# Performance work log

Measured on AMD Instinct MI355X. Metric: run time of the kernel, lower is better.

## Reference

```python
import jax, jax.numpy as jnp
import numpy as np

N = 20000          # nodes
E = 200000         # edges
IN = 256           # in_channels
OUT = 256          # out_channels (heads * per-head)
H = 2              # heads
C = OUT // 2       # per-head channels (out_channels // 2)
TDIM = 100         # time_enc.out_channels
MSG = 156          # msg_dim
EDGE_DIM = TDIM + MSG  # 256
P = 0.1            # dropout prob


def setup_inputs() -> dict:
    key = jax.random.key(0)
    ks = jax.random.split(key, 20)
    s = 1.0 / np.sqrt(IN)
    se = 1.0 / np.sqrt(EDGE_DIM)
    return {
        "x": jax.random.normal(ks[0], (N, IN), jnp.float32),
        "last_update": jax.random.uniform(ks[1], (N,), jnp.float32) * 100.0,
        "edge_index": jax.random.randint(ks[2], (2, E), 0, N, jnp.int64),
        "t": jax.random.uniform(ks[3], (E,), jnp.float32) * 100.0,
        "msg": jax.random.normal(ks[4], (E, MSG), jnp.float32),
        "u_edge": jax.random.uniform(ks[5], (E,), jnp.float32),
        "u_attn": jax.random.uniform(ks[6], (E, H), jnp.float32),
        # TimeEncoder: cos(Linear(1, TDIM))
        "time_w": jax.random.normal(ks[7], (TDIM,), jnp.float32),
        "time_b": jax.random.normal(ks[8], (TDIM,), jnp.float32) * 0.1,
        # TransformerConv params ([in, out] layout)
        "Wq": jax.random.normal(ks[9], (IN, H * C), jnp.float32) * s,
        "bq": jnp.zeros((H * C,), jnp.float32),
        "Wk": jax.random.normal(ks[10], (IN, H * C), jnp.float32) * s,
        "bk": jnp.zeros((H * C,), jnp.float32),
        "Wv": jax.random.normal(ks[11], (IN, H * C), jnp.float32) * s,
        "bv": jnp.zeros((H * C,), jnp.float32),
        "We": jax.random.normal(ks[12], (EDGE_DIM, H * C), jnp.float32) * se,
        "be": jnp.zeros((H * C,), jnp.float32),
        "Ws": jax.random.normal(ks[13], (IN, H * C), jnp.float32) * s,
        "bs": jnp.zeros((H * C,), jnp.float32),
    }


def reference(x, last_update, edge_index, t, msg, u_edge, u_attn,
              time_w, time_b, Wq, bq, Wk, bk, Wv, bv, We, be, Ws, bs):
    src, dst = edge_index[0], edge_index[1]
    # time encoding of relative time (TGN TimeEncoder: cos(Linear(1, TDIM)))
    rel_t = last_update[src] - t                              # [E]
    rel_enc = jnp.cos(rel_t[:, None] * time_w[None, :] + time_b)  # [E, TDIM]
    edge_attr = jnp.concatenate([rel_enc, msg], axis=-1)      # [E, EDGE_DIM]
    # dropout_adj: drop edges with prob P (no rescale)
    keep = u_edge > P                                         # [E] bool

    q = (x @ Wq + bq).reshape(N, H, C)
    k = (x @ Wk + bk).reshape(N, H, C)
    v = (x @ Wv + bv).reshape(N, H, C)
    e = (edge_attr @ We + be).reshape(E, H, C)

    kj = k[src] + e                                           # [E, H, C]
    alpha = jnp.einsum('ehc,ehc->eh', q[dst], kj) / jnp.sqrt(jnp.float32(C))
    alpha = jnp.where(keep[:, None], alpha, -jnp.inf)
    # segment softmax over incoming edges of each dst node
    m = jax.ops.segment_max(alpha, dst, num_segments=N)       # [N, H]
    m = jnp.where(jnp.isfinite(m), m, 0.0)
    ex = jnp.where(keep[:, None], jnp.exp(alpha - m[dst]), 0.0)
    denom = jax.ops.segment_sum(ex, dst, num_segments=N)      # [N, H]
    attn = ex / (denom[dst] + 1e-16)                          # [E, H]
    # attention dropout (post-softmax, inverted scaling)
    attn = attn * (u_attn > P).astype(attn.dtype) / (1.0 - P)

    msg_out = (v[src] + e) * attn[:, :, None]                 # [E, H, C]
    out = jax.ops.segment_sum(msg_out, dst, num_segments=N).reshape(N, H * C)
    # root/skip connection
    return out + (x @ Ws + bs)
```

## Files before the change

### kernel.cpp

```cpp
#include <hip/hip_runtime.h>

#define NND 20000
#define NE 200000
#define PDROP 0.1f

typedef unsigned short u16;
typedef __bf16 bf16x8 __attribute__((ext_vector_type(8)));
typedef float f32x4 __attribute__((ext_vector_type(4)));

__device__ __forceinline__ float b2f(u16 u) {
  unsigned v = ((unsigned)u) << 16;
  float f;
  __builtin_memcpy(&f, &v, 4);
  return f;
}
__device__ __forceinline__ u16 f2b(float f) {
  unsigned x;
  __builtin_memcpy(&x, &f, 4);
  unsigned r = x + 0x7fffu + ((x >> 16) & 1u);
  return (u16)(r >> 16);
}

__global__ void convert_x(const float* __restrict__ x, u16* __restrict__ xb) {
  int i = blockIdx.x * blockDim.x + threadIdx.x;
  if (i < NND * 256 / 4) {
    float4 v = ((const float4*)x)[i];
    ushort4 o;
    o.x = f2b(v.x); o.y = f2b(v.y); o.z = f2b(v.z); o.w = f2b(v.w);
    ((ushort4*)xb)[i] = o;
  }
}

struct WTArgs {
  const float* W[6];
  u16* WT[6];
};
__global__ void convert_wT(WTArgs a) {
  int gid = blockIdx.x * blockDim.x + threadIdx.x;
  if (gid >= 6 * 65536) return;
  int w = gid >> 16, r = gid & 65535;
  if (w < 5) {
    int n = r >> 8, k = r & 255;
    a.WT[w][n * 256 + k] = f2b(a.W[w][k * 256 + n]);
  } else {
    a.WT[5][r] = f2b(a.W[5][r]);
  }
}

__global__ void build_relt(const float* __restrict__ last_update,
                           const int* __restrict__ ei, const float* __restrict__ t,
                           float* __restrict__ relt) {
  int e = blockIdx.x * blockDim.x + threadIdx.x;
  if (e < NE) relt[e] = last_update[ei[e]] - t[e];
}

__global__ void zero2(int* __restrict__ cnt, int* __restrict__ cur) {
  int i = blockIdx.x * blockDim.x + threadIdx.x;
  if (i < NND) { cnt[i] = 0; cur[i] = 0; }
}
__global__ void csr_count(const int* __restrict__ ei, int* __restrict__ cnt) {
  int e = blockIdx.x * blockDim.x + threadIdx.x;
  if (e < NE) atomicAdd(&cnt[ei[NE + e]], 1);
}
__global__ __launch_bounds__(1024) void scan_rowptr(const int* __restrict__ cnt,
                                                    int* __restrict__ rowptr) {
  __shared__ int sums[1024];
  const int tid = threadIdx.x;
  const int base = tid * 20;
  int local[20];
  int run = 0;
#pragma unroll
  for (int i = 0; i < 20; i++) {
    int idx = base + i;
    local[i] = run;
    run += (idx < NND) ? cnt[idx] : 0;
  }
  sums[tid] = run;
  __syncthreads();
  for (int off = 1; off < 1024; off <<= 1) {
    int v = (tid >= off) ? sums[tid - off] : 0;
    __syncthreads();
    sums[tid] += v;
    __syncthreads();
  }
  int prev = (tid > 0) ? sums[tid - 1] : 0;
#pragma unroll
  for (int i = 0; i < 20; i++) {
    int idx = base + i;
    if (idx < NND) rowptr[idx] = prev + local[i];
  }
  if (tid == 1023) rowptr[NND] = sums[1023];
}
__global__ void csr_fill(const int* __restrict__ ei, const int* __restrict__ rowptr,
                         int* __restrict__ cur, int* __restrict__ elist) {
  int e = blockIdx.x * blockDim.x + threadIdx.x;
  if (e < NE) {
    int d = ei[NE + e];
    int pos = rowptr[d] + atomicAdd(&cur[d], 1);
    elist[pos] = e;
  }
}

__device__ __forceinline__ void mfma_tile(const u16 (*As)[72], const u16 (*Bs)[72],
                                          f32x4 acc[4][4], int wm, int wn,
                                          int fr, int fg) {
#pragma unroll
  for (int ks = 0; ks < 2; ks++) {
    bf16x8 a[4], b[4];
#pragma unroll
    for (int i = 0; i < 4; i++)
      a[i] = *(const bf16x8*)&As[wm * 64 + i * 16 + fr][ks * 32 + fg * 8];
#pragma unroll
    for (int j = 0; j < 4; j++)
      b[j] = *(const bf16x8*)&Bs[wn * 64 + j * 16 + fr][ks * 32 + fg * 8];
#pragma unroll
    for (int i = 0; i < 4; i++)
#pragma unroll
      for (int j = 0; j < 4; j++)
        acc[i][j] = __builtin_amdgcn_mfma_f32_16x16x32_bf16(a[i], b[j], acc[i][j], 0, 0, 0);
  }
}

struct NodeArgs {
  const u16* BT[4];
  const float* bias[4];
  u16* outb[3];
  float* outf;
};
__global__ __launch_bounds__(256) void gemm_node(const u16* __restrict__ xb,
                                                 NodeArgs args) {
  __shared__ __attribute__((aligned(16))) u16 As[128][72];
  __shared__ __attribute__((aligned(16))) u16 Bs[128][72];
  const int tid = threadIdx.x;
  const int w = blockIdx.y >> 1;
  const int col0 = (blockIdx.y & 1) * 128;
  const int row0 = blockIdx.x * 128;
  const u16* BT = args.BT[w];
  const float* bias = args.bias[w];
  const int wid = tid >> 6, lane = tid & 63;
  const int wm = wid >> 1, wn = wid & 1;
  const int fr = lane & 15, fg = lane >> 4;
  f32x4 acc[4][4] = {};
  for (int k0 = 0; k0 < 256; k0 += 64) {
#pragma unroll
    for (int i = 0; i < 4; i++) {
      int idx = tid + i * 256;
      int row = idx >> 3, vc = idx & 7;
      int g = row0 + row;
      uint4 v = make_uint4(0, 0, 0, 0);
      if (g < NND) v = *(const uint4*)&xb[(size_t)g * 256 + k0 + vc * 8];
      *(uint4*)&As[row][vc * 8] = v;
      *(uint4*)&Bs[row][vc * 8] = *(const uint4*)&BT[(size_t)(col0 + row) * 256 + k0 + vc * 8];
    }
    __syncthreads();
    mfma_tile(As, Bs, acc, wm, wn, fr, fg);
    __syncthreads();
  }
#pragma unroll
  for (int mi = 0; mi < 4; mi++) {
#pragma unroll
    for (int rr = 0; rr < 4; rr++) {
      int grow = row0 + wm * 64 + mi * 16 + fg * 4 + rr;
      if (grow >= NND) continue;
#pragma unroll
      for (int ni = 0; ni < 4; ni++) {
        int gcol = col0 + wn * 64 + ni * 16 + fr;
        float val = acc[mi][ni][rr] + bias[gcol];
        if (w < 3)
          args.outb[w][(size_t)grow * 256 + gcol] = f2b(val);
        else
          args.outf[(size_t)grow * 256 + gcol] = val;
      }
    }
  }
}

__global__ __launch_bounds__(256) void gemm_qwe(const u16* __restrict__ qb,
                                                const u16* __restrict__ Web,
                                                u16* __restrict__ qWeb) {
  __shared__ __attribute__((aligned(16))) u16 As[128][72];
  __shared__ __attribute__((aligned(16))) u16 Bs[128][72];
  const int tid = threadIdx.x;
  const int h = blockIdx.y >> 1;
  const int col0 = (blockIdx.y & 1) * 128;
  const int row0 = blockIdx.x * 128;
  const int wid = tid >> 6, lane = tid & 63;
  const int wm = wid >> 1, wn = wid & 1;
  const int fr = lane & 15, fg = lane >> 4;
  f32x4 acc[4][4] = {};
  for (int k0 = 0; k0 < 128; k0 += 64) {
#pragma unroll
    for (int i = 0; i < 4; i++) {
      int idx = tid + i * 256;
      int row = idx >> 3, vc = idx & 7;
      int g = row0 + row;
      uint4 v = make_uint4(0, 0, 0, 0);
      if (g < NND) v = *(const uint4*)&qb[(size_t)g * 256 + h * 128 + k0 + vc * 8];
      *(uint4*)&As[row][vc * 8] = v;
      *(uint4*)&Bs[row][vc * 8] =
          *(const uint4*)&Web[(size_t)(col0 + row) * 256 + h * 128 + k0 + vc * 8];
    }
    __syncthreads();
    mfma_tile(As, Bs, acc, wm, wn, fr, fg);
    __syncthreads();
  }
#pragma unroll
  for (int mi = 0; mi < 4; mi++) {
#pragma unroll
    for (int rr = 0; rr < 4; rr++) {
      int grow = row0 + wm * 64 + mi * 16 + fg * 4 + rr;
      if (grow >= NND) continue;
#pragma unroll
      for (int ni = 0; ni < 4; ni++) {
        int gj = col0 + wn * 64 + ni * 16 + fr;
        qWeb[(size_t)grow * 512 + h * 256 + gj] = f2b(acc[mi][ni][rr]);
      }
    }
  }
}

__global__ __launch_bounds__(256) void node_fused(
    const u16* __restrict__ qb, const u16* __restrict__ kb,
    const u16* __restrict__ vb, const u16* __restrict__ qWeb,
    const int* __restrict__ ei, const int* __restrict__ rowptr,
    const int* __restrict__ elist, const float* __restrict__ relt,
    const float* __restrict__ msg, const float* __restrict__ tw,
    const float* __restrict__ tb, const float* __restrict__ be,
    const float* __restrict__ u_edge, const float* __restrict__ u_attn,
    float* __restrict__ alphabuf, u16* __restrict__ aggb,
    float* __restrict__ out) {
  const int node = (blockIdx.x * blockDim.x + threadIdx.x) >> 6;
  const int lane = threadIdx.x & 63;
  const int c0 = lane * 4;
  const int hl = lane >> 5;
  const int beg = rowptr[node], end = rowptr[node + 1];

  ushort4 q4 = *(const ushort4*)&qb[(size_t)node * 256 + c0];
  float qf0 = b2f(q4.x), qf1 = b2f(q4.y), qf2 = b2f(q4.z), qf3 = b2f(q4.w);
  ushort4 w0v = *(const ushort4*)&qWeb[(size_t)node * 512 + c0];
  ushort4 w1v = *(const ushort4*)&qWeb[(size_t)node * 512 + 256 + c0];
  float qw00 = b2f(w0v.x), qw01 = b2f(w0v.y), qw02 = b2f(w0v.z), qw03 = b2f(w0v.w);
  float qw10 = b2f(w1v.x), qw11 = b2f(w1v.y), qw12 = b2f(w1v.z), qw13 = b2f(w1v.w);
  float4 bev = *(const float4*)&be[c0];
  float pb = qf0 * bev.x + qf1 * bev.y + qf2 * bev.z + qf3 * bev.w;
#pragma unroll
  for (int off = 16; off; off >>= 1) pb += __shfl_xor(pb, off);
  float tw0 = 0, tw1 = 0, tw2 = 0, tw3 = 0, tb0 = 0, tb1 = 0, tb2 = 0, tb3 = 0;
  if (c0 < 100) {
    float4 a = *(const float4*)&tw[c0];
    float4 b = *(const float4*)&tb[c0];
    tw0 = a.x; tw1 = a.y; tw2 = a.z; tw3 = a.w;
    tb0 = b.x; tb1 = b.y; tb2 = b.z; tb3 = b.w;
  }
  const float inv = 0.08838834764831845f;

  float m = -INFINITY;
  for (int j = beg; j < end; ++j) {
    int eid = elist[j];
    int s = ei[eid];
    float rt = relt[eid];
    ushort4 k4 = *(const ushort4*)&kb[(size_t)s * 256 + c0];
    float pqk = qf0 * b2f(k4.x) + qf1 * b2f(k4.y) + qf2 * b2f(k4.z) + qf3 * b2f(k4.w);
    float ea0, ea1, ea2, ea3;
    if (c0 < 100) {
      ea0 = __cosf(rt * tw0 + tb0); ea1 = __cosf(rt * tw1 + tb1);
      ea2 = __cosf(rt * tw2 + tb2); ea3 = __cosf(rt * tw3 + tb3);
    } else {
      float4 mm = *(const float4*)&msg[(size_t)eid * 156 + (c0 - 100)];
      ea0 = mm.x; ea1 = mm.y; ea2 = mm.z; ea3 = mm.w;
    }
    float pe0 = qw00 * ea0 + qw01 * ea1 + qw02 * ea2 + qw03 * ea3;
    float pe1 = qw10 * ea0 + qw11 * ea1 + qw12 * ea2 + qw13 * ea3;
    float y0 = pe0 + __shfl_xor(pe0, 32);
    float y1 = pe1 + __shfl_xor(pe1, 32);
    float z = (lane < 32) ? y0 : y1;
#pragma unroll
    for (int off = 16; off; off >>= 1) {
      z += __shfl_xor(z, off);
      pqk += __shfl_xor(pqk, off);
    }
    bool keep = u_edge[eid] > PDROP;
    float a = keep ? (pqk + z + pb) * inv : -INFINITY;
    m = fmaxf(m, a);
    alphabuf[2 * j + hl] = a;
  }

  float den = 0.f, sw = 0.f;
  float vc0 = 0, vc1 = 0, vc2 = 0, vc3 = 0;
  float g00 = 0, g01 = 0, g02 = 0, g03 = 0;
  float g10 = 0, g11 = 0, g12 = 0, g13 = 0;
  for (int j = beg; j < end; ++j) {
    int eid = elist[j];
    float a = alphabuf[2 * j + hl];
    float ex = (a > -1e30f) ? __expf(a - m) : 0.f;
    den += ex;
    float wa = ex * ((u_attn[(size_t)eid * 2 + hl] > PDROP) ? (1.f / 0.9f) : 0.f);
    float wo = __shfl_xor(wa, 32);
    float w0 = (lane < 32) ? wa : wo;
    float w1 = (lane < 32) ? wo : wa;
    if (w0 + w1 != 0.f) {
      int s = ei[eid];
      float rt = relt[eid];
      ushort4 v4 = *(const ushort4*)&vb[(size_t)s * 256 + c0];
      float ea0, ea1, ea2, ea3;
      if (c0 < 100) {
        ea0 = __cosf(rt * tw0 + tb0); ea1 = __cosf(rt * tw1 + tb1);
        ea2 = __cosf(rt * tw2 + tb2); ea3 = __cosf(rt * tw3 + tb3);
      } else {
        float4 mm = *(const float4*)&msg[(size_t)eid * 156 + (c0 - 100)];
        ea0 = mm.x; ea1 = mm.y; ea2 = mm.z; ea3 = mm.w;
      }
      vc0 += wa * b2f(v4.x); vc1 += wa * b2f(v4.y);
      vc2 += wa * b2f(v4.z); vc3 += wa * b2f(v4.w);
      g00 += w0 * ea0; g01 += w0 * ea1; g02 += w0 * ea2; g03 += w0 * ea3;
      g10 += w1 * ea0; g11 += w1 * ea1; g12 += w1 * ea2; g13 += w1 * ea3;
      sw += wa;
    }
  }
  float rden = 1.f / (den + 1e-16f);
  float ro = __shfl_xor(rden, 32);
  float r0 = (lane < 32) ? rden : ro;
  float r1 = (lane < 32) ? ro : rden;
  float4 o = *(float4*)&out[(size_t)node * 256 + c0];
  o.x += (vc0 + sw * bev.x) * rden;
  o.y += (vc1 + sw * bev.y) * rden;
  o.z += (vc2 + sw * bev.z) * rden;
  o.w += (vc3 + sw * bev.w) * rden;
  *(float4*)&out[(size_t)node * 256 + c0] = o;
  ushort4 a0, a1;
  a0.x = f2b(g00 * r0); a0.y = f2b(g01 * r0); a0.z = f2b(g02 * r0); a0.w = f2b(g03 * r0);
  a1.x = f2b(g10 * r1); a1.y = f2b(g11 * r1); a1.z = f2b(g12 * r1); a1.w = f2b(g13 * r1);
  *(ushort4*)&aggb[(size_t)node * 256 + c0] = a0;
  *(ushort4*)&aggb[(size_t)(NND + node) * 256 + c0] = a1;
}

__global__ __launch_bounds__(256) void gemm_final(const u16* __restrict__ aggb,
                                                  const u16* __restrict__ WeT,
                                                  float* __restrict__ out) {
  __shared__ __attribute__((aligned(16))) u16 As[128][72];
  __shared__ __attribute__((aligned(16))) u16 Bs[128][72];
  const int tid = threadIdx.x;
  const int h = blockIdx.y;
  const int row0 = blockIdx.x * 128;
  const u16* A = aggb + (size_t)h * NND * 256;
  const int wid = tid >> 6, lane = tid & 63;
  const int wm = wid >> 1, wn = wid & 1;
  const int fr = lane & 15, fg = lane >> 4;
  f32x4 acc[4][4] = {};
  for (int k0 = 0; k0 < 256; k0 += 64) {
#pragma unroll
    for (int i = 0; i < 4; i++) {
      int idx = tid + i * 256;
      int row = idx >> 3, vc = idx & 7;
      int g = row0 + row;
      uint4 v = make_uint4(0, 0, 0, 0);
      if (g < NND) v = *(const uint4*)&A[(size_t)g * 256 + k0 + vc * 8];
      *(uint4*)&As[row][vc * 8] = v;
      *(uint4*)&Bs[row][vc * 8] =
          *(const uint4*)&WeT[(size_t)(h * 128 + row) * 256 + k0 + vc * 8];
    }
    __syncthreads();
    mfma_tile(As, Bs, acc, wm, wn, fr, fg);
    __syncthreads();
  }
#pragma unroll
  for (int mi = 0; mi < 4; mi++) {
#pragma unroll
    for (int rr = 0; rr < 4; rr++) {
      int grow = row0 + wm * 64 + mi * 16 + fg * 4 + rr;
      if (grow >= NND) continue;
#pragma unroll
      for (int ni = 0; ni < 4; ni++) {
        int gcol = wn * 64 + ni * 16 + fr;
        out[(size_t)grow * 256 + h * 128 + gcol] += acc[mi][ni][rr];
      }
    }
  }
}

extern "C" void kernel_launch(void* const* d_in, const int* in_sizes, int n_in,
                              void* d_out, int out_size, void* d_ws, size_t ws_size,
                              hipStream_t stream) {
  const float* x = (const float*)d_in[0];
  const float* last_update = (const float*)d_in[1];
  const int* ei = (const int*)d_in[2];
  const float* t = (const float*)d_in[3];
  const float* msg = (const float*)d_in[4];
  const float* u_edge = (const float*)d_in[5];
  const float* u_attn = (const float*)d_in[6];
  const float* time_w = (const float*)d_in[7];
  const float* time_b = (const float*)d_in[8];
  const float* Wq = (const float*)d_in[9];
  const float* bq = (const float*)d_in[10];
  const float* Wk = (const float*)d_in[11];
  const float* bk = (const float*)d_in[12];
  const float* Wv = (const float*)d_in[13];
  const float* bv = (const float*)d_in[14];
  const float* We = (const float*)d_in[15];
  const float* be = (const float*)d_in[16];
  const float* Ws = (const float*)d_in[17];
  const float* bs = (const float*)d_in[18];
  float* out = (float*)d_out;

  char* ws = (char*)d_ws;
  u16* xb = (u16*)(ws + 0);
  u16* WT0 = (u16*)(ws + 10240000);
  float* relt = (float*)(ws + 11026432);
  u16* qb = (u16*)(ws + 11826432);
  u16* kb = (u16*)(ws + 22066432);
  u16* vb = (u16*)(ws + 32306432);
  u16* qWeb = (u16*)(ws + 42546432);
  u16* aggb = (u16*)(ws + 63026432);
  float* alphabuf = (float*)(ws + 83506432);
  int* cnt = (int*)(ws + 85106432);
  int* cur = (int*)(ws + 85186432);
  int* rowptr = (int*)(ws + 85266432);
  int* elist = (int*)(ws + 85346448);

  zero2<<<(NND + 255) / 256, 256, 0, stream>>>(cnt, cur);
  csr_count<<<(NE + 255) / 256, 256, 0, stream>>>(ei, cnt);
  scan_rowptr<<<1, 1024, 0, stream>>>(cnt, rowptr);
  csr_fill<<<(NE + 255) / 256, 256, 0, stream>>>(ei, rowptr, cur, elist);

  WTArgs wa;
  wa.W[0] = Wq; wa.W[1] = Wk; wa.W[2] = Wv; wa.W[3] = Ws; wa.W[4] = We; wa.W[5] = We;
  for (int i = 0; i < 6; i++) wa.WT[i] = WT0 + (size_t)i * 65536;
  convert_wT<<<(6 * 65536 + 255) / 256, 256, 0, stream>>>(wa);
  convert_x<<<(NND * 64 + 255) / 256, 256, 0, stream>>>(x, xb);
  build_relt<<<(NE + 255) / 256, 256, 0, stream>>>(last_update, ei, t, relt);

  NodeArgs na;
  na.BT[0] = wa.WT[0]; na.BT[1] = wa.WT[1]; na.BT[2] = wa.WT[2]; na.BT[3] = wa.WT[3];
  na.bias[0] = bq; na.bias[1] = bk; na.bias[2] = bv; na.bias[3] = bs;
  na.outb[0] = qb; na.outb[1] = kb; na.outb[2] = vb;
  na.outf = out;
  dim3 gn((NND + 127) / 128, 8);
  gemm_node<<<gn, 256, 0, stream>>>(xb, na);

  dim3 gq((NND + 127) / 128, 4);
  gemm_qwe<<<gq, 256, 0, stream>>>(qb, wa.WT[5], qWeb);

  node_fused<<<NND / 4, 256, 0, stream>>>(qb, kb, vb, qWeb, ei, rowptr, elist,
                                          relt, msg, time_w, time_b, be, u_edge,
                                          u_attn, alphabuf, aggb, out);

  dim3 gf((NND + 127) / 128, 2);
  gemm_final<<<gf, 256, 0, stream>>>(aggb, wa.WT[4], out);
}
```

Before: 286.9 us.

## Split node-fused attention into edge-parallel alpha kernel and node aggregation

Replaces the per-node fused kernel with an edge-parallel kernel that computes attention logits one wavefront per edge and scatters them, along with dropout masks, relative time and source ids, into CSR order. A node-level kernel then does the segment softmax and aggregation from these compacted arrays and reads a bf16 copy of msg. The aim is to remove the load imbalance and serial per-node logit loop of the old kernel and to make the aggregation reads contiguous. In exchange it adds an extra kernel launch, extra workspace traffic for the scattered arrays and the bf16 msg copy, and bf16 rounding of msg.

```diff
diff --git a/kernel.cpp b/kernel.cpp
--- a/kernel.cpp
+++ b/kernel.cpp
@@ -47,13 +47,6 @@
   }
 }
 
-__global__ void build_relt(const float* __restrict__ last_update,
-                           const int* __restrict__ ei, const float* __restrict__ t,
-                           float* __restrict__ relt) {
-  int e = blockIdx.x * blockDim.x + threadIdx.x;
-  if (e < NE) relt[e] = last_update[ei[e]] - t[e];
-}
-
 __global__ void zero2(int* __restrict__ cnt, int* __restrict__ cur) {
   int i = blockIdx.x * blockDim.x + threadIdx.x;
   if (i < NND) { cnt[i] = 0; cur[i] = 0; }
@@ -92,12 +85,14 @@
   if (tid == 1023) rowptr[NND] = sums[1023];
 }
 __global__ void csr_fill(const int* __restrict__ ei, const int* __restrict__ rowptr,
-                         int* __restrict__ cur, int* __restrict__ elist) {
+                         int* __restrict__ cur, int* __restrict__ elist,
+                         int* __restrict__ pos) {
   int e = blockIdx.x * blockDim.x + threadIdx.x;
   if (e < NE) {
     int d = ei[NE + e];
-    int pos = rowptr[d] + atomicAdd(&cur[d], 1);
-    elist[pos] = e;
+    int p = rowptr[d] + atomicAdd(&cur[d], 1);
+    elist[p] = e;
+    pos[e] = p;
   }
 }
 
@@ -219,117 +214,139 @@
   }
 }
 
-__global__ __launch_bounds__(256) void node_fused(
+__global__ __launch_bounds__(256) void edge_alpha(
     const u16* __restrict__ qb, const u16* __restrict__ kb,
-    const u16* __restrict__ vb, const u16* __restrict__ qWeb,
-    const int* __restrict__ ei, const int* __restrict__ rowptr,
-    const int* __restrict__ elist, const float* __restrict__ relt,
+    const u16* __restrict__ qWeb, const int* __restrict__ ei,
+    const float* __restrict__ last_update, const float* __restrict__ t,
     const float* __restrict__ msg, const float* __restrict__ tw,
-    const float* __restrict__ tb, const float* __restrict__ be,
+    const float* __restrict__ tb_, const float* __restrict__ be,
     const float* __restrict__ u_edge, const float* __restrict__ u_attn,
-    float* __restrict__ alphabuf, u16* __restrict__ aggb,
+    const int* __restrict__ pos, float2* __restrict__ alpha2,
+    float2* __restrict__ wm2, float* __restrict__ reltc,
+    int* __restrict__ srcc, u16* __restrict__ msgb) {
+  int e = (blockIdx.x * blockDim.x + threadIdx.x) >> 6;
+  int lane = threadIdx.x & 63;
+  if (e >= NE) return;
+  int c0 = lane * 4;
+  int s = ei[e], d = ei[NE + e];
+  float rt = last_update[s] - t[e];
+  ushort4 q4 = *(const ushort4*)&qb[(size_t)d * 256 + c0];
+  ushort4 k4 = *(const ushort4*)&kb[(size_t)s * 256 + c0];
+  float4 bev = *(const float4*)&be[c0];
+  float pqk = b2f(q4.x) * (b2f(k4.x) + bev.x) + b2f(q4.y) * (b2f(k4.y) + bev.y) +
+              b2f(q4.z) * (b2f(k4.z) + bev.z) + b2f(q4.w) * (b2f(k4.w) + bev.w);
+  float ea0, ea1, ea2, ea3;
+  if (c0 < 100) {
+    float4 a = *(const float4*)&tw[c0];
+    float4 b = *(const float4*)&tb_[c0];
+    ea0 = __cosf(rt * a.x + b.x); ea1 = __cosf(rt * a.y + b.y);
+    ea2 = __cosf(rt * a.z + b.z); ea3 = __cosf(rt * a.w + b.w);
+  } else {
+    float4 mm = *(const float4*)&msg[(size_t)e * 156 + (c0 - 100)];
+    ea0 = mm.x; ea1 = mm.y; ea2 = mm.z; ea3 = mm.w;
+    ushort4 mo;
+    mo.x = f2b(ea0); mo.y = f2b(ea1); mo.z = f2b(ea2); mo.w = f2b(ea3);
+    *(ushort4*)&msgb[(size_t)e * 156 + (c0 - 100)] = mo;
+  }
+  ushort4 w0v = *(const ushort4*)&qWeb[(size_t)d * 512 + c0];
+  ushort4 w1v = *(const ushort4*)&qWeb[(size_t)d * 512 + 256 + c0];
+  float pe0 = b2f(w0v.x) * ea0 + b2f(w0v.y) * ea1 + b2f(w0v.z) * ea2 + b2f(w0v.w) * ea3;
+  float pe1 = b2f(w1v.x) * ea0 + b2f(w1v.y) * ea1 + b2f(w1v.z) * ea2 + b2f(w1v.w) * ea3;
+  float y0 = pe0 + __shfl_xor(pe0, 32);
+  float y1 = pe1 + __shfl_xor(pe1, 32);
+  float z = (lane < 32) ? y0 : y1;
+#pragma unroll
+  for (int off = 16; off; off >>= 1) {
+    z += __shfl_xor(z, off);
+    pqk += __shfl_xor(pqk, off);
+  }
+  float a = (pqk + z) * 0.08838834764831845f;
+  if (!(u_edge[e] > PDROP)) a = -INFINITY;
+  float aothr = __shfl_xor(a, 32);
+  if (lane == 0) {
+    int p = pos[e];
+    alpha2[p] = make_float2(a, aothr);
+    float2 ua = *(const float2*)&u_attn[(size_t)e * 2];
+    wm2[p] = make_float2(ua.x > PDROP ? (1.f / 0.9f) : 0.f,
+                         ua.y > PDROP ? (1.f / 0.9f) : 0.f);
+    reltc[p] = rt;
+    srcc[p] = s;
+  }
+}
+
+__global__ __launch_bounds__(256) void node_agg(
+    const u16* __restrict__ vb, const u16* __restrict__ msgb,
+    const float2* __restrict__ alpha2, const float2* __restrict__ wm2,
+    const float* __restrict__ reltc, const int* __restrict__ srcc,
+    const int* __restrict__ elist, const int* __restrict__ rowptr,
+    const float* __restrict__ tw, const float* __restrict__ tb_,
+    const float* __restrict__ be, u16* __restrict__ aggb,
     float* __restrict__ out) {
-  const int node = (blockIdx.x * blockDim.x + threadIdx.x) >> 6;
-  const int lane = threadIdx.x & 63;
-  const int c0 = lane * 4;
-  const int hl = lane >> 5;
+  int node = (blockIdx.x * blockDim.x + threadIdx.x) >> 6;
+  int lane = threadIdx.x & 63;
+  if (node >= NND) return;
   const int beg = rowptr[node], end = rowptr[node + 1];
-
-  ushort4 q4 = *(const ushort4*)&qb[(size_t)node * 256 + c0];
-  float qf0 = b2f(q4.x), qf1 = b2f(q4.y), qf2 = b2f(q4.z), qf3 = b2f(q4.w);
-  ushort4 w0v = *(const ushort4*)&qWeb[(size_t)node * 512 + c0];
-  ushort4 w1v = *(const ushort4*)&qWeb[(size_t)node * 512 + 256 + c0];
-  float qw00 = b2f(w0v.x), qw01 = b2f(w0v.y), qw02 = b2f(w0v.z), qw03 = b2f(w0v.w);
-  float qw10 = b2f(w1v.x), qw11 = b2f(w1v.y), qw12 = b2f(w1v.z), qw13 = b2f(w1v.w);
-  float4 bev = *(const float4*)&be[c0];
-  float pb = qf0 * bev.x + qf1 * bev.y + qf2 * bev.z + qf3 * bev.w;
-#pragma unroll
-  for (int off = 16; off; off >>= 1) pb += __shfl_xor(pb, off);
+  const int c0 = lane * 4, hl = lane >> 5;
   float tw0 = 0, tw1 = 0, tw2 = 0, tw3 = 0, tb0 = 0, tb1 = 0, tb2 = 0, tb3 = 0;
   if (c0 < 100) {
     float4 a = *(const float4*)&tw[c0];
-    float4 b = *(const float4*)&tb[c0];
+    float4 b = *(const float4*)&tb_[c0];
     tw0 = a.x; tw1 = a.y; tw2 = a.z; tw3 = a.w;
     tb0 = b.x; tb1 = b.y; tb2 = b.z; tb3 = b.w;
   }
-  const float inv = 0.08838834764831845f;
-
-  float m = -INFINITY;
+  float4 bev = *(const float4*)&be[c0];
+  float m0 = -INFINITY, m1 = -INFINITY;
   for (int j = beg; j < end; ++j) {
-    int eid = elist[j];
-    int s = ei[eid];
-    float rt = relt[eid];
-    ushort4 k4 = *(const ushort4*)&kb[(size_t)s * 256 + c0];
-    float pqk = qf0 * b2f(k4.x) + qf1 * b2f(k4.y) + qf2 * b2f(k4.z) + qf3 * b2f(k4.w);
-    float ea0, ea1, ea2, ea3;
-    if (c0 < 100) {
-      ea0 = __cosf(rt * tw0 + tb0); ea1 = __cosf(rt * tw1 + tb1);
-      ea2 = __cosf(rt * tw2 + tb2); ea3 = __cosf(rt * tw3 + tb3);
-    } else {
-      float4 mm = *(const float4*)&msg[(size_t)eid * 156 + (c0 - 100)];
-      ea0 = mm.x; ea1 = mm.y; ea2 = mm.z; ea3 = mm.w;
-    }
-    float pe0 = qw00 * ea0 + qw01 * ea1 + qw02 * ea2 + qw03 * ea3;
-    float pe1 = qw10 * ea0 + qw11 * ea1 + qw12 * ea2 + qw13 * ea3;
-    float y0 = pe0 + __shfl_xor(pe0, 32);
-    float y1 = pe1 + __shfl_xor(pe1, 32);
-    float z = (lane < 32) ? y0 : y1;
-#pragma unroll
-    for (int off = 16; off; off >>= 1) {
-      z += __shfl_xor(z, off);
-      pqk += __shfl_xor(pqk, off);
-    }
-    bool keep = u_edge[eid] > PDROP;
-    float a = keep ? (pqk + z + pb) * inv : -INFINITY;
-    m = fmaxf(m, a);
-    alphabuf[2 * j + hl] = a;
-  }
-
-  float den = 0.f, sw = 0.f;
+    float2 a2 = alpha2[j];
+    m0 = fmaxf(m0, a2.x);
+    m1 = fmaxf(m1, a2.y);
+  }
+  float den0 = 0.f, den1 = 0.f, sw0 = 0.f, sw1 = 0.f;
   float vc0 = 0, vc1 = 0, vc2 = 0, vc3 = 0;
   float g00 = 0, g01 = 0, g02 = 0, g03 = 0;
   float g10 = 0, g11 = 0, g12 = 0, g13 = 0;
   for (int j = beg; j < end; ++j) {
-    int eid = elist[j];
-    float a = alphabuf[2 * j + hl];
-    float ex = (a > -1e30f) ? __expf(a - m) : 0.f;
-    den += ex;
-    float wa = ex * ((u_attn[(size_t)eid * 2 + hl] > PDROP) ? (1.f / 0.9f) : 0.f);
-    float wo = __shfl_xor(wa, 32);
-    float w0 = (lane < 32) ? wa : wo;
-    float w1 = (lane < 32) ? wo : wa;
+    float2 a2 = alpha2[j];
+    float ex0 = (a2.x > -1e30f) ? __expf(a2.x - m0) : 0.f;
+    float ex1 = (a2.y > -1e30f) ? __expf(a2.y - m1) : 0.f;
+    den0 += ex0; den1 += ex1;
+    float2 wm = wm2[j];
+    float w0 = ex0 * wm.x, w1 = ex1 * wm.y;
     if (w0 + w1 != 0.f) {
-      int s = ei[eid];
-      float rt = relt[eid];
+      int s = srcc[j];
+      float rt = reltc[j];
       ushort4 v4 = *(const ushort4*)&vb[(size_t)s * 256 + c0];
       float ea0, ea1, ea2, ea3;
       if (c0 < 100) {
         ea0 = __cosf(rt * tw0 + tb0); ea1 = __cosf(rt * tw1 + tb1);
         ea2 = __cosf(rt * tw2 + tb2); ea3 = __cosf(rt * tw3 + tb3);
       } else {
-        float4 mm = *(const float4*)&msg[(size_t)eid * 156 + (c0 - 100)];
-        ea0 = mm.x; ea1 = mm.y; ea2 = mm.z; ea3 = mm.w;
+        int eid = elist[j];
+        ushort4 mm = *(const ushort4*)&msgb[(size_t)eid * 156 + (c0 - 100)];
+        ea0 = b2f(mm.x); ea1 = b2f(mm.y); ea2 = b2f(mm.z); ea3 = b2f(mm.w);
       }
-      vc0 += wa * b2f(v4.x); vc1 += wa * b2f(v4.y);
-      vc2 += wa * b2f(v4.z); vc3 += wa * b2f(v4.w);
+      float wv = hl ? w1 : w0;
+      vc0 += wv * b2f(v4.x); vc1 += wv * b2f(v4.y);
+      vc2 += wv * b2f(v4.z); vc3 += wv * b2f(v4.w);
       g00 += w0 * ea0; g01 += w0 * ea1; g02 += w0 * ea2; g03 += w0 * ea3;
       g10 += w1 * ea0; g11 += w1 * ea1; g12 += w1 * ea2; g13 += w1 * ea3;
-      sw += wa;
-    }
-  }
-  float rden = 1.f / (den + 1e-16f);
-  float ro = __shfl_xor(rden, 32);
-  float r0 = (lane < 32) ? rden : ro;
-  float r1 = (lane < 32) ? ro : rden;
+      sw0 += w0; sw1 += w1;
+    }
+  }
+  float rden0 = 1.f / (den0 + 1e-16f), rden1 = 1.f / (den1 + 1e-16f);
+  float rv = hl ? rden1 : rden0;
+  float swv = hl ? sw1 : sw0;
   float4 o = *(float4*)&out[(size_t)node * 256 + c0];
-  o.x += (vc0 + sw * bev.x) * rden;
-  o.y += (vc1 + sw * bev.y) * rden;
-  o.z += (vc2 + sw * bev.z) * rden;
-  o.w += (vc3 + sw * bev.w) * rden;
+  o.x += (vc0 + swv * bev.x) * rv;
+  o.y += (vc1 + swv * bev.y) * rv;
+  o.z += (vc2 + swv * bev.z) * rv;
+  o.w += (vc3 + swv * bev.w) * rv;
   *(float4*)&out[(size_t)node * 256 + c0] = o;
   ushort4 a0, a1;
-  a0.x = f2b(g00 * r0); a0.y = f2b(g01 * r0); a0.z = f2b(g02 * r0); a0.w = f2b(g03 * r0);
-  a1.x = f2b(g10 * r1); a1.y = f2b(g11 * r1); a1.z = f2b(g12 * r1); a1.w = f2b(g13 * r1);
+  a0.x = f2b(g00 * rden0); a0.y = f2b(g01 * rden0);
+  a0.z = f2b(g02 * rden0); a0.w = f2b(g03 * rden0);
+  a1.x = f2b(g10 * rden1); a1.y = f2b(g11 * rden1);
+  a1.z = f2b(g12 * rden1); a1.w = f2b(g13 * rden1);
   *(ushort4*)&aggb[(size_t)node * 256 + c0] = a0;
   *(ushort4*)&aggb[(size_t)(NND + node) * 256 + c0] = a1;
 }
@@ -405,29 +422,32 @@
   char* ws = (char*)d_ws;
   u16* xb = (u16*)(ws + 0);
   u16* WT0 = (u16*)(ws + 10240000);
-  float* relt = (float*)(ws + 11026432);
-  u16* qb = (u16*)(ws + 11826432);
-  u16* kb = (u16*)(ws + 22066432);
-  u16* vb = (u16*)(ws + 32306432);
-  u16* qWeb = (u16*)(ws + 42546432);
-  u16* aggb = (u16*)(ws + 63026432);
-  float* alphabuf = (float*)(ws + 83506432);
-  int* cnt = (int*)(ws + 85106432);
-  int* cur = (int*)(ws + 85186432);
-  int* rowptr = (int*)(ws + 85266432);
-  int* elist = (int*)(ws + 85346448);
+  u16* qb = (u16*)(ws + 11026432);
+  u16* kb = (u16*)(ws + 21266432);
+  u16* vb = (u16*)(ws + 31506432);
+  u16* qWeb = (u16*)(ws + 41746432);
+  u16* aggb = (u16*)(ws + 62226432);
+  float2* alpha2 = (float2*)(ws + 82706432);
+  float2* wm2 = (float2*)(ws + 84306432);
+  float* reltc = (float*)(ws + 85906432);
+  int* srcc = (int*)(ws + 86706432);
+  int* pos = (int*)(ws + 87506432);
+  int* elist = (int*)(ws + 88306432);
+  u16* msgb = (u16*)(ws + 89106432);
+  int* cnt = (int*)(ws + 151506432);
+  int* cur = (int*)(ws + 151586432);
+  int* rowptr = (int*)(ws + 151666432);
 
   zero2<<<(NND + 255) / 256, 256, 0, stream>>>(cnt, cur);
   csr_count<<<(NE + 255) / 256, 256, 0, stream>>>(ei, cnt);
   scan_rowptr<<<1, 1024, 0, stream>>>(cnt, rowptr);
-  csr_fill<<<(NE + 255) / 256, 256, 0, stream>>>(ei, rowptr, cur, elist);
+  csr_fill<<<(NE + 255) / 256, 256, 0, stream>>>(ei, rowptr, cur, elist, pos);
 
   WTArgs wa;
   wa.W[0] = Wq; wa.W[1] = Wk; wa.W[2] = Wv; wa.W[3] = Ws; wa.W[4] = We; wa.W[5] = We;
   for (int i = 0; i < 6; i++) wa.WT[i] = WT0 + (size_t)i * 65536;
   convert_wT<<<(6 * 65536 + 255) / 256, 256, 0, stream>>>(wa);
   convert_x<<<(NND * 64 + 255) / 256, 256, 0, stream>>>(x, xb);
-  build_relt<<<(NE + 255) / 256, 256, 0, stream>>>(last_update, ei, t, relt);
 
   NodeArgs na;
   na.BT[0] = wa.WT[0]; na.BT[1] = wa.WT[1]; na.BT[2] = wa.WT[2]; na.BT[3] = wa.WT[3];
@@ -440,9 +460,13 @@
   dim3 gq((NND + 127) / 128, 4);
   gemm_qwe<<<gq, 256, 0, stream>>>(qb, wa.WT[5], qWeb);
 
-  node_fused<<<NND / 4, 256, 0, stream>>>(qb, kb, vb, qWeb, ei, rowptr, elist,
-                                          relt, msg, time_w, time_b, be, u_edge,
-                                          u_attn, alphabuf, aggb, out);
+  edge_alpha<<<(NE + 3) / 4, 256, 0, stream>>>(
+      qb, kb, qWeb, ei, last_update, t, msg, time_w, time_b, be, u_edge,
+      u_attn, pos, alpha2, wm2, reltc, srcc, msgb);
+
+  node_agg<<<(NND + 3) / 4, 256, 0, stream>>>(
+      vb, msgb, alpha2, wm2, reltc, srcc, elist, rowptr, time_w, time_b, be,
+      aggb, out);
 
   dim3 gf((NND + 127) / 128, 2);
   gemm_final<<<gf, 256, 0, stream>>>(aggb, wa.WT[4], out);
```

Result: slower. 333.1 us (+16.1%).

## Fuse two-pass segment softmax into single online-softmax pass and inline rel_t

Applied to the files above, without the earlier changes.

Replaces the two-pass per-node softmax (score pass writing alphabuf, then a weighted-accumulate pass re-reading edges) with a single online-softmax loop that rescales the running accumulators whenever the per-head max grows. The edge's time-encoding cos values and msg loads are now computed once instead of twice, the alphabuf round-trip is removed, and the build_relt kernel is dropped by computing last_update[src]-t inline. In exchange, every edge now loads v and u_attn even when it is dropped, and the loop does extra exp and rescale work.

```diff
diff --git a/kernel.cpp b/kernel.cpp
--- a/kernel.cpp
+++ b/kernel.cpp
@@ -47,13 +47,6 @@
   }
 }
 
-__global__ void build_relt(const float* __restrict__ last_update,
-                           const int* __restrict__ ei, const float* __restrict__ t,
-                           float* __restrict__ relt) {
-  int e = blockIdx.x * blockDim.x + threadIdx.x;
-  if (e < NE) relt[e] = last_update[ei[e]] - t[e];
-}
-
 __global__ void zero2(int* __restrict__ cnt, int* __restrict__ cur) {
   int i = blockIdx.x * blockDim.x + threadIdx.x;
   if (i < NND) { cnt[i] = 0; cur[i] = 0; }
@@ -96,8 +89,8 @@
   int e = blockIdx.x * blockDim.x + threadIdx.x;
   if (e < NE) {
     int d = ei[NE + e];
-    int pos = rowptr[d] + atomicAdd(&cur[d], 1);
-    elist[pos] = e;
+    int p = rowptr[d] + atomicAdd(&cur[d], 1);
+    elist[p] = e;
   }
 }
 
@@ -222,18 +215,18 @@
 __global__ __launch_bounds__(256) void node_fused(
     const u16* __restrict__ qb, const u16* __restrict__ kb,
     const u16* __restrict__ vb, const u16* __restrict__ qWeb,
-    const int* __restrict__ ei, const int* __restrict__ rowptr,
-    const int* __restrict__ elist, const float* __restrict__ relt,
-    const float* __restrict__ msg, const float* __restrict__ tw,
-    const float* __restrict__ tb, const float* __restrict__ be,
-    const float* __restrict__ u_edge, const float* __restrict__ u_attn,
-    float* __restrict__ alphabuf, u16* __restrict__ aggb,
+    const int* __restrict__ ei, const float* __restrict__ last_update,
+    const float* __restrict__ t, const float* __restrict__ msg,
+    const float* __restrict__ tw, const float* __restrict__ tb_,
+    const float* __restrict__ be, const float* __restrict__ u_edge,
+    const float* __restrict__ u_attn, const int* __restrict__ rowptr,
+    const int* __restrict__ elist, u16* __restrict__ aggb,
     float* __restrict__ out) {
   const int node = (blockIdx.x * blockDim.x + threadIdx.x) >> 6;
   const int lane = threadIdx.x & 63;
-  const int c0 = lane * 4;
-  const int hl = lane >> 5;
+  if (node >= NND) return;
   const int beg = rowptr[node], end = rowptr[node + 1];
+  const int c0 = lane * 4, hl = lane >> 5;
 
   ushort4 q4 = *(const ushort4*)&qb[(size_t)node * 256 + c0];
   float qf0 = b2f(q4.x), qf1 = b2f(q4.y), qf2 = b2f(q4.z), qf3 = b2f(q4.w);
@@ -248,19 +241,26 @@
   float tw0 = 0, tw1 = 0, tw2 = 0, tw3 = 0, tb0 = 0, tb1 = 0, tb2 = 0, tb3 = 0;
   if (c0 < 100) {
     float4 a = *(const float4*)&tw[c0];
-    float4 b = *(const float4*)&tb[c0];
+    float4 b = *(const float4*)&tb_[c0];
     tw0 = a.x; tw1 = a.y; tw2 = a.z; tw3 = a.w;
     tb0 = b.x; tb1 = b.y; tb2 = b.z; tb3 = b.w;
   }
   const float inv = 0.08838834764831845f;
 
-  float m = -INFINITY;
+  float m0 = -INFINITY, m1 = -INFINITY;
+  float den0 = 0.f, den1 = 0.f, sw0 = 0.f, sw1 = 0.f;
+  float vc0 = 0, vc1 = 0, vc2 = 0, vc3 = 0;
+  float g00 = 0, g01 = 0, g02 = 0, g03 = 0;
+  float g10 = 0, g11 = 0, g12 = 0, g13 = 0;
+
   for (int j = beg; j < end; ++j) {
     int eid = elist[j];
     int s = ei[eid];
-    float rt = relt[eid];
+    float rt = last_update[s] - t[eid];
     ushort4 k4 = *(const ushort4*)&kb[(size_t)s * 256 + c0];
-    float pqk = qf0 * b2f(k4.x) + qf1 * b2f(k4.y) + qf2 * b2f(k4.z) + qf3 * b2f(k4.w);
+    ushort4 v4 = *(const ushort4*)&vb[(size_t)s * 256 + c0];
+    bool keep = u_edge[eid] > PDROP;
+    float2 ua = *(const float2*)&u_attn[(size_t)eid * 2];
     float ea0, ea1, ea2, ea3;
     if (c0 < 100) {
       ea0 = __cosf(rt * tw0 + tb0); ea1 = __cosf(rt * tw1 + tb1);
@@ -269,6 +269,7 @@
       float4 mm = *(const float4*)&msg[(size_t)eid * 156 + (c0 - 100)];
       ea0 = mm.x; ea1 = mm.y; ea2 = mm.z; ea3 = mm.w;
     }
+    float pqk = qf0 * b2f(k4.x) + qf1 * b2f(k4.y) + qf2 * b2f(k4.z) + qf3 * b2f(k4.w);
     float pe0 = qw00 * ea0 + qw01 * ea1 + qw02 * ea2 + qw03 * ea3;
     float pe1 = qw10 * ea0 + qw11 * ea1 + qw12 * ea2 + qw13 * ea3;
     float y0 = pe0 + __shfl_xor(pe0, 32);
@@ -279,59 +280,55 @@
       z += __shfl_xor(z, off);
       pqk += __shfl_xor(pqk, off);
     }
-    bool keep = u_edge[eid] > PDROP;
     float a = keep ? (pqk + z + pb) * inv : -INFINITY;
-    m = fmaxf(m, a);
-    alphabuf[2 * j + hl] = a;
-  }
-
-  float den = 0.f, sw = 0.f;
-  float vc0 = 0, vc1 = 0, vc2 = 0, vc3 = 0;
-  float g00 = 0, g01 = 0, g02 = 0, g03 = 0;
-  float g10 = 0, g11 = 0, g12 = 0, g13 = 0;
-  for (int j = beg; j < end; ++j) {
-    int eid = elist[j];
-    float a = alphabuf[2 * j + hl];
-    float ex = (a > -1e30f) ? __expf(a - m) : 0.f;
-    den += ex;
-    float wa = ex * ((u_attn[(size_t)eid * 2 + hl] > PDROP) ? (1.f / 0.9f) : 0.f);
-    float wo = __shfl_xor(wa, 32);
-    float w0 = (lane < 32) ? wa : wo;
-    float w1 = (lane < 32) ? wo : wa;
-    if (w0 + w1 != 0.f) {
-      int s = ei[eid];
-      float rt = relt[eid];
-      ushort4 v4 = *(const ushort4*)&vb[(size_t)s * 256 + c0];
-      float ea0, ea1, ea2, ea3;
-      if (c0 < 100) {
-        ea0 = __cosf(rt * tw0 + tb0); ea1 = __cosf(rt * tw1 + tb1);
-        ea2 = __cosf(rt * tw2 + tb2); ea3 = __cosf(rt * tw3 + tb3);
-      } else {
-        float4 mm = *(const float4*)&msg[(size_t)eid * 156 + (c0 - 100)];
-        ea0 = mm.x; ea1 = mm.y; ea2 = mm.z; ea3 = mm.w;
-      }
-      vc0 += wa * b2f(v4.x); vc1 += wa * b2f(v4.y);
-      vc2 += wa * b2f(v4.z); vc3 += wa * b2f(v4.w);
-      g00 += w0 * ea0; g01 += w0 * ea1; g02 += w0 * ea2; g03 += w0 * ea3;
-      g10 += w1 * ea0; g11 += w1 * ea1; g12 += w1 * ea2; g13 += w1 * ea3;
-      sw += wa;
-    }
-  }
-  float rden = 1.f / (den + 1e-16f);
-  float ro = __shfl_xor(rden, 32);
-  float r0 = (lane < 32) ? rden : ro;
-  float r1 = (lane < 32) ? ro : rden;
+    float aoth = __shfl_xor(a, 32);
+    float a0 = (lane < 32) ? a : aoth;
+    float a1 = (lane < 32) ? aoth : a;
+    if (a0 > m0) {
+      float sc = (m0 > -1e30f) ? __expf(m0 - a0) : 0.f;
+      den0 *= sc; sw0 *= sc;
+      g00 *= sc; g01 *= sc; g02 *= sc; g03 *= sc;
+      float scv = hl ? 1.f : sc;
+      vc0 *= scv; vc1 *= scv; vc2 *= scv; vc3 *= scv;
+      m0 = a0;
+    }
+    if (a1 > m1) {
+      float sc = (m1 > -1e30f) ? __expf(m1 - a1) : 0.f;
+      den1 *= sc; sw1 *= sc;
+      g10 *= sc; g11 *= sc; g12 *= sc; g13 *= sc;
+      float scv = hl ? sc : 1.f;
+      vc0 *= scv; vc1 *= scv; vc2 *= scv; vc3 *= scv;
+      m1 = a1;
+    }
+    float ex0 = (a0 > -1e30f) ? __expf(a0 - m0) : 0.f;
+    float ex1 = (a1 > -1e30f) ? __expf(a1 - m1) : 0.f;
+    den0 += ex0; den1 += ex1;
+    float w0 = ex0 * ((ua.x > PDROP) ? (1.f / 0.9f) : 0.f);
+    float w1 = ex1 * ((ua.y > PDROP) ? (1.f / 0.9f) : 0.f);
+    float wv = hl ? w1 : w0;
+    vc0 += wv * b2f(v4.x); vc1 += wv * b2f(v4.y);
+    vc2 += wv * b2f(v4.z); vc3 += wv * b2f(v4.w);
+    g00 += w0 * ea0; g01 += w0 * ea1; g02 += w0 * ea2; g03 += w0 * ea3;
+    g10 += w1 * ea0; g11 += w1 * ea1; g12 += w1 * ea2; g13 += w1 * ea3;
+    sw0 += w0; sw1 += w1;
+  }
+
+  float rden0 = 1.f / (den0 + 1e-16f), rden1 = 1.f / (den1 + 1e-16f);
+  float rv = hl ? rden1 : rden0;
+  float swv = hl ? sw1 : sw0;
   float4 o = *(float4*)&out[(size_t)node * 256 + c0];
-  o.x += (vc0 + sw * bev.x) * rden;
-  o.y += (vc1 + sw * bev.y) * rden;
-  o.z += (vc2 + sw * bev.z) * rden;
-  o.w += (vc3 + sw * bev.w) * rden;
+  o.x += (vc0 + swv * bev.x) * rv;
+  o.y += (vc1 + swv * bev.y) * rv;
+  o.z += (vc2 + swv * bev.z) * rv;
+  o.w += (vc3 + swv * bev.w) * rv;
   *(float4*)&out[(size_t)node * 256 + c0] = o;
-  ushort4 a0, a1;
-  a0.x = f2b(g00 * r0); a0.y = f2b(g01 * r0); a0.z = f2b(g02 * r0); a0.w = f2b(g03 * r0);
-  a1.x = f2b(g10 * r1); a1.y = f2b(g11 * r1); a1.z = f2b(g12 * r1); a1.w = f2b(g13 * r1);
-  *(ushort4*)&aggb[(size_t)node * 256 + c0] = a0;
-  *(ushort4*)&aggb[(size_t)(NND + node) * 256 + c0] = a1;
+  ushort4 a0v, a1v;
+  a0v.x = f2b(g00 * rden0); a0v.y = f2b(g01 * rden0);
+  a0v.z = f2b(g02 * rden0); a0v.w = f2b(g03 * rden0);
+  a1v.x = f2b(g10 * rden1); a1v.y = f2b(g11 * rden1);
+  a1v.z = f2b(g12 * rden1); a1v.w = f2b(g13 * rden1);
+  *(ushort4*)&aggb[(size_t)node * 256 + c0] = a0v;
+  *(ushort4*)&aggb[(size_t)(NND + node) * 256 + c0] = a1v;
 }
 
 __global__ __launch_bounds__(256) void gemm_final(const u16* __restrict__ aggb,
@@ -405,17 +402,15 @@
   char* ws = (char*)d_ws;
   u16* xb = (u16*)(ws + 0);
   u16* WT0 = (u16*)(ws + 10240000);
-  float* relt = (float*)(ws + 11026432);
-  u16* qb = (u16*)(ws + 11826432);
-  u16* kb = (u16*)(ws + 22066432);
-  u16* vb = (u16*)(ws + 32306432);
-  u16* qWeb = (u16*)(ws + 42546432);
-  u16* aggb = (u16*)(ws + 63026432);
-  float* alphabuf = (float*)(ws + 83506432);
-  int* cnt = (int*)(ws + 85106432);
-  int* cur = (int*)(ws + 85186432);
-  int* rowptr = (int*)(ws + 85266432);
-  int* elist = (int*)(ws + 85346448);
+  u16* qb = (u16*)(ws + 11026432);
+  u16* kb = (u16*)(ws + 21266432);
+  u16* vb = (u16*)(ws + 31506432);
+  u16* qWeb = (u16*)(ws + 41746432);
+  u16* aggb = (u16*)(ws + 62226432);
+  int* cnt = (int*)(ws + 82706432);
+  int* cur = (int*)(ws + 82786432);
+  int* rowptr = (int*)(ws + 82866432);
+  int* elist = (int*)(ws + 82946448);
 
   zero2<<<(NND + 255) / 256, 256, 0, stream>>>(cnt, cur);
   csr_count<<<(NE + 255) / 256, 256, 0, stream>>>(ei, cnt);
@@ -427,7 +422,6 @@
   for (int i = 0; i < 6; i++) wa.WT[i] = WT0 + (size_t)i * 65536;
   convert_wT<<<(6 * 65536 + 255) / 256, 256, 0, stream>>>(wa);
   convert_x<<<(NND * 64 + 255) / 256, 256, 0, stream>>>(x, xb);
-  build_relt<<<(NE + 255) / 256, 256, 0, stream>>>(last_update, ei, t, relt);
 
   NodeArgs na;
   na.BT[0] = wa.WT[0]; na.BT[1] = wa.WT[1]; na.BT[2] = wa.WT[2]; na.BT[3] = wa.WT[3];
@@ -440,9 +434,9 @@
   dim3 gq((NND + 127) / 128, 4);
   gemm_qwe<<<gq, 256, 0, stream>>>(qb, wa.WT[5], qWeb);
 
-  node_fused<<<NND / 4, 256, 0, stream>>>(qb, kb, vb, qWeb, ei, rowptr, elist,
-                                          relt, msg, time_w, time_b, be, u_edge,
-                                          u_attn, alphabuf, aggb, out);
+  node_fused<<<(NND + 3) / 4, 256, 0, stream>>>(
+      qb, kb, vb, qWeb, ei, last_update, t, msg, time_w, time_b, be, u_edge,
+      u_attn, rowptr, elist, aggb, out);
 
   dim3 gf((NND + 127) / 128, 2);
   gemm_final<<<gf, 256, 0, stream>>>(aggb, wa.WT[4], out);
```

Measured after the change: 238.4 us. -16.9%, faster.
